# Performance work log

Hardware: AMD Instinct MI355X
Metric: run time of the kernel (lower is better)

Reference implementation:

```python
import jax, jax.numpy as jnp
import numpy as np

H = 512; W = 512; C = 32; B = 2; N = 120000; HEADS = 2; HD = C // HEADS; S = 9
INDEX_SHIFT = jnp.array([[0,0],[-1,0],[1,0],[0,1],[-1,1],[1,1],[0,-1],[-1,-1],[1,-1]], dtype=jnp.int32)


def setup_inputs() -> dict:
    key = jax.random.key(0)
    ks = jax.random.split(key, 20)
    bev_feats = jax.random.normal(ks[0], (B, N, C), jnp.float32)
    coors = []
    for b in range(B):
        perm = jax.random.permutation(ks[1 + b], H * W)[:N]
        coors.append(jnp.stack([perm // W, perm % W], axis=-1))
    bev_coors = jnp.stack(coors).astype(jnp.int32)
    s = 1.0 / np.sqrt(C)
    u = lambda k, shape, lim: jax.random.uniform(k, shape, jnp.float32, -lim, lim)
    return {
        'bev_feats': bev_feats,
        'bev_coors': bev_coors,
        'ln_w': jnp.ones((C,), jnp.float32),
        'ln_b': jnp.zeros((C,), jnp.float32),
        'wq': u(ks[3], (C, C), s), 'bq': u(ks[4], (C,), s),
        'wk': u(ks[5], (C, C), s), 'bk': u(ks[6], (C,), s),
        'wv': u(ks[7], (C, C), s), 'bv': u(ks[8], (C,), s),
        'pos_w': u(ks[9], (C, 2), 1.0 / np.sqrt(2.0)), 'pos_b': u(ks[10], (C,), 1.0 / np.sqrt(2.0)),
        'in_w': u(ks[11], (3 * C, C), s), 'in_b': jnp.zeros((3 * C,), jnp.float32),
        'out_w': u(ks[12], (C, C), s), 'out_b': jnp.zeros((C,), jnp.float32),
    }


def reference(bev_feats, bev_coors, ln_w, ln_b, wq, bq, wk, bk, wv, bv, pos_w, pos_b, in_w, in_b, out_w, out_b):
    def single(feats, coors):
        # LayerNorm (biased var, eps=1e-5)
        mu = feats.mean(-1, keepdims=True)
        var = feats.var(-1, keepdims=True)
        x = (feats - mu) / jnp.sqrt(var + 1e-5) * ln_w + ln_b
        # qkv 1x1 conv == linear
        q = x @ wq.T + bq
        k = x @ wk.T + bk
        v = x @ wv.T + bv
        # dense grid lookup: coord -> voxel index (-1 if empty)
        flat0 = coors[:, 0] * W + coors[:, 1]
        grid = jnp.full((H * W,), -1, jnp.int32).at[flat0].set(jnp.arange(N, dtype=jnp.int32))
        sc = coors[None] + INDEX_SHIFT[:, None]                      # [9,N,2]
        valid = (sc[..., 0] >= 0) & (sc[..., 0] < H) & (sc[..., 1] >= 0) & (sc[..., 1] < W)
        flat = jnp.clip(sc[..., 0], 0, H - 1) * W + jnp.clip(sc[..., 1], 0, W - 1)
        idx = jnp.where(valid, grid[flat], -1)                       # [9,N]
        pos = INDEX_SHIFT.astype(x.dtype) @ pos_w.T + pos_b          # [9,C]
        m = (idx >= 0)[..., None]
        tv = jnp.where(m, v[idx] + pos[:, None, :], 0.0)             # [9,N,C]
        tk = jnp.where(m, k[idx], 0.0)
        keyt = jnp.swapaxes(tk, 0, 1)                                # [N,9,C]
        valt = jnp.swapaxes(tv, 0, 1)
        # tiny MHA: query len 1, kv len 9, 2 heads (dropout inactive at eval)
        qp = q @ in_w[:C].T + in_b[:C]
        kp = keyt @ in_w[C:2 * C].T + in_b[C:2 * C]
        vp = valt @ in_w[2 * C:].T + in_b[2 * C:]
        qh = qp.reshape(N, HEADS, HD)
        kh = kp.reshape(N, S, HEADS, HD)
        vh = vp.reshape(N, S, HEADS, HD)
        attn = jax.nn.softmax(jnp.einsum('nhd,nshd->nhs', qh, kh) / np.sqrt(HD), axis=-1)
        o = jnp.einsum('nhs,nshd->nhd', attn, vh).reshape(N, C)
        o = o @ out_w.T + out_b
        # scatter to pseudo image [C,H,W]
        canvas = jnp.zeros((C, H * W), o.dtype).at[:, flat0].set(o.T)
        return canvas.reshape(C, H, W)
    return jax.vmap(single)(bev_feats, bev_coors)
```

## Files before the change

### kernel.cpp

```cpp
#include <hip/hip_runtime.h>
#include <hip/hip_fp16.h>
#include <cstdio>
#include <cstdint>

#define HH 512
#define WW 512
#define CC 32
#define BB 2
#define NN 120000
#define HWPIX (HH*WW)
#define NPTS (BB*NN)
#define NPIX (BB*HWPIX)
#define NBLK (NPIX/256)

__device__ __forceinline__ void h8_to_f8(float4 raw, float* o) {
    const __half2* h = (const __half2*)&raw;
    #pragma unroll
    for (int i = 0; i < 4; ++i) {
        float2 f = __half22float2(h[i]);
        o[2 * i] = f.x; o[2 * i + 1] = f.y;
    }
}

__global__ __launch_bounds__(256) void prep(const float* __restrict__ wq, const float* __restrict__ wk,
                          const float* __restrict__ wv, const float* __restrict__ in_w,
                          const float* __restrict__ out_w,
                          const float* __restrict__ bq, const float* __restrict__ bk,
                          const float* __restrict__ bv, const float* __restrict__ in_b,
                          const float* __restrict__ pos_w, const float* __restrict__ pos_b,
                          float* __restrict__ M, float* __restrict__ V, int* __restrict__ cnt) {
    int blk = blockIdx.x;
    if (blk < 16) {
        int tid = blk * 256 + threadIdx.x;
        int which = tid >> 10;
        int e = tid & 1023;
        int cp = e & 31;
        int j  = e >> 5;
        if (which < 3) {
            const float* w = (which == 0) ? wq : ((which == 1) ? wk : wv);
            const float* Wrow = in_w + (which * 32 + cp) * 32;
            float acc = 0.f;
            #pragma unroll
            for (int t = 0; t < 32; ++t) acc += Wrow[t] * w[t * 32 + j];
            M[which * 1024 + j * 32 + cp] = acc;
        } else {
            M[3 * 1024 + j * 32 + cp] = out_w[cp * 32 + j];
        }
    } else if (blk == 16) {
        int tid = threadIdx.x;
        if (tid < 32) {
            float a = 0.f, b = 0.f, c = 0.f;
            #pragma unroll
            for (int t = 0; t < 32; ++t) {
                a += in_w[tid * 32 + t] * bq[t];
                b += in_w[(32 + tid) * 32 + t] * bk[t];
                c += in_w[(64 + tid) * 32 + t] * bv[t];
            }
            V[tid]      = a + in_b[tid];
            V[32 + tid] = b;
            V[64 + tid] = c;
        } else if (tid < 128) {
            int grp = (tid - 32) >> 5;
            int cp  = tid & 31;
            float acc = 0.f;
            #pragma unroll
            for (int t = 0; t < 32; ++t) {
                float src = (grp == 0) ? pos_w[t * 2 + 0] : ((grp == 1) ? pos_w[t * 2 + 1] : pos_b[t]);
                acc += in_w[(64 + cp) * 32 + t] * src;
            }
            V[96 + grp * 32 + cp] = acc;
        }
    } else {
        for (int i = threadIdx.x; i < 2048; i += 256) cnt[i] = 0;
    }
}

__global__ void build_grid(const int* __restrict__ coors, int* __restrict__ grid,
                           int* __restrict__ cnt) {
    int P = blockIdx.x * blockDim.x + threadIdx.x;
    if (P >= NPTS) return;
    int b = P / NN;
    int n = P - b * NN;
    int y = coors[P * 2 + 0];
    int x = coors[P * 2 + 1];
    int pix = b * HWPIX + y * WW + x;
    grid[pix] = n;
    atomicAdd(&cnt[pix >> 8], 1);
}

__global__ __launch_bounds__(256) void scan2048(const int* __restrict__ cnt, int* __restrict__ off) {
    __shared__ int ps[256];
    int tid = threadIdx.x;
    int v[8], loc[8];
    int t = 0;
    #pragma unroll
    for (int k = 0; k < 8; ++k) { v[k] = cnt[tid * 8 + k]; loc[k] = t; t += v[k]; }
    ps[tid] = t;
    __syncthreads();
    for (int d = 1; d < 256; d <<= 1) {
        int val = ps[tid];
        int add = (tid >= d) ? ps[tid - d] : 0;
        __syncthreads();
        ps[tid] = val + add;
        __syncthreads();
    }
    int excl = (tid > 0) ? ps[tid - 1] : 0;
    #pragma unroll
    for (int k = 0; k < 8; ++k) off[tid * 8 + k] = excl + loc[k];
}

__global__ __launch_bounds__(256) void assign_ranks(const int* __restrict__ off,
                                                    int* __restrict__ grid,
                                                    int* __restrict__ rmap) {
    __shared__ int woff[4];
    int tid = threadIdx.x;
    int pix = blockIdx.x * 256 + tid;
    int n = grid[pix];
    bool occ = n >= 0;
    unsigned long long mask = __ballot(occ);
    int lane = tid & 63, wvi = tid >> 6;
    if (lane == 0) woff[wvi] = __popcll(mask);
    __syncthreads();
    int pre = 0;
    for (int w = 0; w < wvi; ++w) pre += woff[w];
    if (occ) {
        int r = off[blockIdx.x] + pre + __popcll(mask & ((1ull << lane) - 1ull));
        grid[pix] = r;
        rmap[(pix >> 18) * NN + n] = r;
    }
}

__global__ __launch_bounds__(128) void stage1(const float* __restrict__ feats,
                                              const float* __restrict__ ln_w,
                                              const float* __restrict__ ln_b,
                                              const float* __restrict__ M,
                                              const float* __restrict__ V,
                                              const int* __restrict__ rmap,
                                              __half* __restrict__ qh,
                                              __half* __restrict__ kvh) {
    int gp = blockIdx.x * 128 + threadIdx.x;
    int r = rmap[gp];

    const float* fr = feats + ((size_t)gp << 5);
    float x[32];
    #pragma unroll
    for (int k = 0; k < 8; ++k) ((float4*)x)[k] = ((const float4*)fr)[k];

    float s1 = 0.f, s2 = 0.f;
    #pragma unroll
    for (int j = 0; j < 32; ++j) { s1 += x[j]; s2 += x[j] * x[j]; }
    float mu   = s1 * (1.f / 32.f);
    float var  = s2 * (1.f / 32.f) - mu * mu;
    float rstd = rsqrtf(var + 1e-5f);
    #pragma unroll
    for (int j = 0; j < 32; ++j) x[j] = (x[j] - mu) * rstd * ln_w[j] + ln_b[j];

    float acc[32];
    __half2 hbuf[16];

    #pragma unroll
    for (int c = 0; c < 32; ++c) acc[c] = V[c];
    #pragma unroll
    for (int j = 0; j < 32; ++j) {
        float xv = x[j];
        #pragma unroll
        for (int c = 0; c < 32; ++c) acc[c] += xv * M[j * 32 + c];
    }
    #pragma unroll
    for (int c = 0; c < 16; ++c) hbuf[c] = __floats2half2_rn(acc[2 * c], acc[2 * c + 1]);
    {
        float4* qd = (float4*)(qh + ((size_t)r << 5));
        #pragma unroll
        for (int k = 0; k < 4; ++k) qd[k] = ((float4*)hbuf)[k];
    }

    __half2 kvbuf[32];

    #pragma unroll
    for (int c = 0; c < 32; ++c) acc[c] = V[32 + c];
    #pragma unroll
    for (int j = 0; j < 32; ++j) {
        float xv = x[j];
        #pragma unroll
        for (int c = 0; c < 32; ++c) acc[c] += xv * M[1024 + j * 32 + c];
    }
    #pragma unroll
    for (int c = 0; c < 16; ++c) kvbuf[c] = __floats2half2_rn(acc[2 * c], acc[2 * c + 1]);

    #pragma unroll
    for (int c = 0; c < 32; ++c) acc[c] = V[64 + c];
    #pragma unroll
    for (int j = 0; j < 32; ++j) {
        float xv = x[j];
        #pragma unroll
        for (int c = 0; c < 32; ++c) acc[c] += xv * M[2048 + j * 32 + c];
    }
    #pragma unroll
    for (int c = 0; c < 16; ++c) kvbuf[16 + c] = __floats2half2_rn(acc[2 * c], acc[2 * c + 1]);

    float4* kd = (float4*)(kvh + ((size_t)r << 6));
    #pragma unroll
    for (int k = 0; k < 8; ++k) kd[k] = ((float4*)kvbuf)[k];
}

__global__ __launch_bounds__(256) void stage23(const int* __restrict__ grid,
                                               const __half* __restrict__ qh,
                                               const __half* __restrict__ kvh,
                                               const float* __restrict__ M,
                                               const float* __restrict__ V,
                                               const float* __restrict__ in_b,
                                               const float* __restrict__ out_b,
                                               float* __restrict__ out) {
    __shared__ __half2 lso[256 * 17];
    __shared__ int lsr[256], lsp[256];
    __shared__ int woff[4];

    int w = (blockIdx.x & 7) * 256 + (blockIdx.x >> 3);
    int tid = threadIdx.x;
    int pix = w * 256 + tid;

    int rk = grid[pix];
    bool occ = rk >= 0;
    unsigned long long mask = __ballot(occ);
    int lane = tid & 63, wvi = tid >> 6;
    if (lane == 0) woff[wvi] = __popcll(mask);
    __syncthreads();
    int pre = 0;
    for (int ww = 0; ww < wvi; ++ww) pre += woff[ww];
    int cnt = woff[0] + woff[1] + woff[2] + woff[3];
    int slot = -1;
    if (occ) {
        slot = pre + __popcll(mask & ((1ull << lane) - 1ull));
        lsr[slot] = rk;
        lsp[slot] = tid;
    }
    __syncthreads();

    const int DYC[9] = {0,-1,1,0,-1,1,0,-1,1};
    const int DXC[9] = {0,0,0,1,1,1,-1,-1,-1};

    if (tid < cnt) {
        int i = tid;
        int r = lsr[i];
        int pixl = w * 256 + lsp[i];
        int b = pixl >> 18;
        int p = pixl & (HWPIX - 1);
        int y = p >> 9, x = p & 511;

        float qf[32];
        {
            const float4* q4 = (const float4*)(qh + ((size_t)r << 5));
            float4 r0 = q4[0], r1 = q4[1], r2 = q4[2], r3 = q4[3];
            h8_to_f8(r0, qf); h8_to_f8(r1, qf + 8); h8_to_f8(r2, qf + 16); h8_to_f8(r3, qf + 24);
        }

        int nr[9];
        #pragma unroll
        for (int s = 0; s < 9; ++s) {
            int sy = y + DYC[s], sx = x + DXC[s];
            nr[s] = (sy >= 0 && sy < HH && sx >= 0 && sx < WW) ? grid[(b << 18) + (sy << 9) + sx] : -1;
        }

        float eb0 = 0.f, eb1 = 0.f;
        #pragma unroll
        for (int c = 0; c < 16; ++c) {
            eb0 += qf[c]      * in_b[32 + c];
            eb1 += qf[16 + c] * in_b[48 + c];
        }

        float lg0[9], lg1[9];
        #pragma unroll
        for (int s = 0; s < 9; ++s) {
            float d0 = eb0, d1 = eb1;
            if (nr[s] >= 0) {
                const float4* kp = (const float4*)(kvh + ((size_t)nr[s] << 6));
                float kf[32];
                h8_to_f8(kp[0], kf);      h8_to_f8(kp[1], kf + 8);
                h8_to_f8(kp[2], kf + 16); h8_to_f8(kp[3], kf + 24);
                #pragma unroll
                for (int c = 0; c < 16; ++c) {
                    d0 += qf[c]      * kf[c];
                    d1 += qf[16 + c] * kf[16 + c];
                }
            }
            lg0[s] = d0 * 0.25f;
            lg1[s] = d1 * 0.25f;
        }
        float m0 = lg0[0], m1 = lg1[0];
        #pragma unroll
        for (int s = 1; s < 9; ++s) { m0 = fmaxf(m0, lg0[s]); m1 = fmaxf(m1, lg1[s]); }
        float l0 = 0.f, l1 = 0.f;
        #pragma unroll
        for (int s = 0; s < 9; ++s) {
            lg0[s] = __expf(lg0[s] - m0); l0 += lg0[s];
            lg1[s] = __expf(lg1[s] - m1); l1 += lg1[s];
        }

        float o[32];
        #pragma unroll
        for (int c = 0; c < 32; ++c) o[c] = 0.f;
        float wdy0 = 0.f, wdx0 = 0.f, woc0 = 0.f;
        float wdy1 = 0.f, wdx1 = 0.f, woc1 = 0.f;
        #pragma unroll
        for (int s = 0; s < 9; ++s) {
            if (nr[s] >= 0) {
                float w0 = lg0[s], w1 = lg1[s];
                const float4* vp = (const float4*)(kvh + ((size_t)nr[s] << 6)) + 4;
                float vf[32];
                h8_to_f8(vp[0], vf);      h8_to_f8(vp[1], vf + 8);
                h8_to_f8(vp[2], vf + 16); h8_to_f8(vp[3], vf + 24);
                #pragma unroll
                for (int c = 0; c < 16; ++c) {
                    o[c]      += w0 * vf[c];
                    o[16 + c] += w1 * vf[16 + c];
                }
                wdy0 += w0 * (float)DYC[s]; wdx0 += w0 * (float)DXC[s]; woc0 += w0;
                wdy1 += w1 * (float)DYC[s]; wdx1 += w1 * (float)DXC[s]; woc1 += w1;
            }
        }
        float rl0 = 1.f / l0, rl1 = 1.f / l1;
        #pragma unroll
        for (int c = 0; c < 16; ++c) {
            o[c]      = (o[c]      + wdy0 * V[96 + c]      + wdx0 * V[128 + c]      + woc0 * V[160 + c])      * rl0 + in_b[64 + c];
            o[16 + c] = (o[16 + c] + wdy1 * V[96 + 16 + c] + wdx1 * V[128 + 16 + c] + woc1 * V[160 + 16 + c]) * rl1 + in_b[80 + c];
        }

        float acc[32];
        #pragma unroll
        for (int c = 0; c < 32; ++c) acc[c] = out_b[c];
        #pragma unroll
        for (int j = 0; j < 32; ++j) {
            float vj = o[j];
            #pragma unroll
            for (int c = 0; c < 32; ++c) acc[c] += vj * M[3072 + j * 32 + c];
        }

        __half2* lrow = lso + i * 17;
        #pragma unroll
        for (int c = 0; c < 16; ++c) lrow[c] = __floats2half2_rn(acc[2 * c], acc[2 * c + 1]);
    }
    __syncthreads();

    int b = pix >> 18;
    int p = pix & (HWPIX - 1);
    float* outb = out + (size_t)b * CC * HWPIX + p;
    if (occ) {
        const __half2* lrow = lso + slot * 17;
        #pragma unroll
        for (int c2 = 0; c2 < 16; ++c2) {
            float2 f = __half22float2(lrow[c2]);
            outb[(2 * c2) * HWPIX]     = f.x;
            outb[(2 * c2 + 1) * HWPIX] = f.y;
        }
    } else {
        #pragma unroll
        for (int cc = 0; cc < 32; ++cc) outb[cc * HWPIX] = 0.f;
    }
}

extern "C" void kernel_launch(void* const* d_in, const int* in_sizes, int n_in,
                              void* d_out, int out_size, void* d_ws, size_t ws_size,
                              hipStream_t stream) {
    const float* feats = (const float*)d_in[0];
    const int*   coors = (const int*)d_in[1];
    const float* ln_w  = (const float*)d_in[2];
    const float* ln_b  = (const float*)d_in[3];
    const float* wq    = (const float*)d_in[4];
    const float* bq    = (const float*)d_in[5];
    const float* wk    = (const float*)d_in[6];
    const float* bk    = (const float*)d_in[7];
    const float* wv    = (const float*)d_in[8];
    const float* bv    = (const float*)d_in[9];
    const float* pos_w = (const float*)d_in[10];
    const float* pos_b = (const float*)d_in[11];
    const float* in_w  = (const float*)d_in[12];
    const float* in_b  = (const float*)d_in[13];
    const float* out_w = (const float*)d_in[14];
    const float* out_b = (const float*)d_in[15];

    int*    grid = (int*)d_ws;
    __half* qh   = (__half*)((int*)d_ws + NPIX);
    __half* kvh  = qh + (size_t)NPTS * 32;
    float*  M    = (float*)(kvh + (size_t)NPTS * 64);
    float*  V    = M + 4096;
    size_t need = (size_t)NPIX * 4 + (size_t)NPTS * 96 * 2 + (4096 + 192) * 4;
    if (ws_size < need) {
        fprintf(stderr, "kernel_launch: ws too small: %zu < %zu\n", ws_size, need);
        return;
    }
    int* cnt  = (int*)d_out + (out_size - 4096);
    int* off  = cnt + 2048;
    int* rmap = (int*)d_out + (out_size - 4096 - NPTS);

    hipMemsetAsync(grid, 0xFF, (size_t)NPIX * sizeof(int), stream);
    prep<<<18, 256, 0, stream>>>(wq, wk, wv, in_w, out_w, bq, bk, bv, in_b, pos_w, pos_b, M, V, cnt);
    build_grid<<<(NPTS + 255) / 256, 256, 0, stream>>>(coors, grid, cnt);
    scan2048<<<1, 256, 0, stream>>>(cnt, off);
    assign_ranks<<<NBLK, 256, 0, stream>>>(off, grid, rmap);
    stage1<<<NPTS / 128, 128, 0, stream>>>(feats, ln_w, ln_b, M, V, rmap, qh, kvh);
    stage23<<<NBLK, 256, 0, stream>>>(grid, qh, kvh, M, V, in_b, out_b, (float*)d_out);
}
```

Baseline: 237.1 us.

## Index q/kv by pixel with a byte occupancy map instead of compacted ranks

Removes the grid build, prefix-scan and rank-assignment kernels and the int grid memset. stage1 now reads coordinates directly and writes q and kv into pixel-indexed buffers, setting a byte occupancy flag per pixel; prep zeroes that flag map. stage23 tests neighbour occupancy with byte loads and fetches neighbour kv rows by pixel address, which keeps spatial neighbours close in memory. In exchange, the q/kv workspace grows to cover every pixel, so the data is sparse and cache lines are less densely used.

```diff
diff --git a/kernel.cpp b/kernel.cpp
--- a/kernel.cpp
+++ b/kernel.cpp
@@ -28,7 +28,7 @@
                           const float* __restrict__ bq, const float* __restrict__ bk,
                           const float* __restrict__ bv, const float* __restrict__ in_b,
                           const float* __restrict__ pos_w, const float* __restrict__ pos_b,
-                          float* __restrict__ M, float* __restrict__ V, int* __restrict__ cnt) {
+                          float* __restrict__ M, float* __restrict__ V, int* __restrict__ fmap_i) {
     int blk = blockIdx.x;
     if (blk < 16) {
         int tid = blk * 256 + threadIdx.x;
@@ -71,75 +71,27 @@
             V[96 + grp * 32 + cp] = acc;
         }
     } else {
-        for (int i = threadIdx.x; i < 2048; i += 256) cnt[i] = 0;
-    }
-}
-
-__global__ void build_grid(const int* __restrict__ coors, int* __restrict__ grid,
-                           int* __restrict__ cnt) {
-    int P = blockIdx.x * blockDim.x + threadIdx.x;
-    if (P >= NPTS) return;
-    int b = P / NN;
-    int n = P - b * NN;
-    int y = coors[P * 2 + 0];
-    int x = coors[P * 2 + 1];
-    int pix = b * HWPIX + y * WW + x;
-    grid[pix] = n;
-    atomicAdd(&cnt[pix >> 8], 1);
-}
-
-__global__ __launch_bounds__(256) void scan2048(const int* __restrict__ cnt, int* __restrict__ off) {
-    __shared__ int ps[256];
-    int tid = threadIdx.x;
-    int v[8], loc[8];
-    int t = 0;
-    #pragma unroll
-    for (int k = 0; k < 8; ++k) { v[k] = cnt[tid * 8 + k]; loc[k] = t; t += v[k]; }
-    ps[tid] = t;
-    __syncthreads();
-    for (int d = 1; d < 256; d <<= 1) {
-        int val = ps[tid];
-        int add = (tid >= d) ? ps[tid - d] : 0;
-        __syncthreads();
-        ps[tid] = val + add;
-        __syncthreads();
-    }
-    int excl = (tid > 0) ? ps[tid - 1] : 0;
-    #pragma unroll
-    for (int k = 0; k < 8; ++k) off[tid * 8 + k] = excl + loc[k];
-}
-
-__global__ __launch_bounds__(256) void assign_ranks(const int* __restrict__ off,
-                                                    int* __restrict__ grid,
-                                                    int* __restrict__ rmap) {
-    __shared__ int woff[4];
-    int tid = threadIdx.x;
-    int pix = blockIdx.x * 256 + tid;
-    int n = grid[pix];
-    bool occ = n >= 0;
-    unsigned long long mask = __ballot(occ);
-    int lane = tid & 63, wvi = tid >> 6;
-    if (lane == 0) woff[wvi] = __popcll(mask);
-    __syncthreads();
-    int pre = 0;
-    for (int w = 0; w < wvi; ++w) pre += woff[w];
-    if (occ) {
-        int r = off[blockIdx.x] + pre + __popcll(mask & ((1ull << lane) - 1ull));
-        grid[pix] = r;
-        rmap[(pix >> 18) * NN + n] = r;
-    }
-}
-
-__global__ __launch_bounds__(128) void stage1(const float* __restrict__ feats,
+        int base = (blk - 17) * 2048 + threadIdx.x * 8;
+        int4 z = {0, 0, 0, 0};
+        *(int4*)(fmap_i + base)     = z;
+        *(int4*)(fmap_i + base + 4) = z;
+    }
+}
+
+__global__ __launch_bounds__(256) void stage1(const float* __restrict__ feats,
+                                              const int* __restrict__ coors,
                                               const float* __restrict__ ln_w,
                                               const float* __restrict__ ln_b,
                                               const float* __restrict__ M,
                                               const float* __restrict__ V,
-                                              const int* __restrict__ rmap,
                                               __half* __restrict__ qh,
-                                              __half* __restrict__ kvh) {
-    int gp = blockIdx.x * 128 + threadIdx.x;
-    int r = rmap[gp];
+                                              __half* __restrict__ kvh,
+                                              unsigned char* __restrict__ fmap) {
+    int gp = blockIdx.x * 256 + threadIdx.x;
+    if (gp >= NPTS) return;
+    int b = (gp >= NN) ? 1 : 0;
+    int2 yx = ((const int2*)coors)[gp];
+    int pix = (b << 18) + (yx.x << 9) + yx.y;
 
     const float* fr = feats + ((size_t)gp << 5);
     float x[32];
@@ -169,7 +121,7 @@
     #pragma unroll
     for (int c = 0; c < 16; ++c) hbuf[c] = __floats2half2_rn(acc[2 * c], acc[2 * c + 1]);
     {
-        float4* qd = (float4*)(qh + ((size_t)r << 5));
+        float4* qd = (float4*)(qh + ((size_t)pix << 5));
         #pragma unroll
         for (int k = 0; k < 4; ++k) qd[k] = ((float4*)hbuf)[k];
     }
@@ -198,12 +150,14 @@
     #pragma unroll
     for (int c = 0; c < 16; ++c) kvbuf[16 + c] = __floats2half2_rn(acc[2 * c], acc[2 * c + 1]);
 
-    float4* kd = (float4*)(kvh + ((size_t)r << 6));
+    float4* kd = (float4*)(kvh + ((size_t)pix << 6));
     #pragma unroll
     for (int k = 0; k < 8; ++k) kd[k] = ((float4*)kvbuf)[k];
-}
-
-__global__ __launch_bounds__(256) void stage23(const int* __restrict__ grid,
+
+    fmap[pix] = 1;
+}
+
+__global__ __launch_bounds__(256) void stage23(const unsigned char* __restrict__ fmap,
                                                const __half* __restrict__ qh,
                                                const __half* __restrict__ kvh,
                                                const float* __restrict__ M,
@@ -212,15 +166,14 @@
                                                const float* __restrict__ out_b,
                                                float* __restrict__ out) {
     __shared__ __half2 lso[256 * 17];
-    __shared__ int lsr[256], lsp[256];
+    __shared__ int lsp[256];
     __shared__ int woff[4];
 
     int w = (blockIdx.x & 7) * 256 + (blockIdx.x >> 3);
     int tid = threadIdx.x;
     int pix = w * 256 + tid;
 
-    int rk = grid[pix];
-    bool occ = rk >= 0;
+    bool occ = fmap[pix] != 0;
     unsigned long long mask = __ballot(occ);
     int lane = tid & 63, wvi = tid >> 6;
     if (lane == 0) woff[wvi] = __popcll(mask);
@@ -231,7 +184,6 @@
     int slot = -1;
     if (occ) {
         slot = pre + __popcll(mask & ((1ull << lane) - 1ull));
-        lsr[slot] = rk;
         lsp[slot] = tid;
     }
     __syncthreads();
@@ -240,25 +192,27 @@
     const int DXC[9] = {0,0,0,1,1,1,-1,-1,-1};
 
     if (tid < cnt) {
-        int i = tid;
-        int r = lsr[i];
-        int pixl = w * 256 + lsp[i];
+        int pixl = w * 256 + lsp[tid];
         int b = pixl >> 18;
         int p = pixl & (HWPIX - 1);
         int y = p >> 9, x = p & 511;
 
         float qf[32];
         {
-            const float4* q4 = (const float4*)(qh + ((size_t)r << 5));
+            const float4* q4 = (const float4*)(qh + ((size_t)pixl << 5));
             float4 r0 = q4[0], r1 = q4[1], r2 = q4[2], r3 = q4[3];
             h8_to_f8(r0, qf); h8_to_f8(r1, qf + 8); h8_to_f8(r2, qf + 16); h8_to_f8(r3, qf + 24);
         }
 
-        int nr[9];
+        int np[9];
+        bool nv[9];
         #pragma unroll
         for (int s = 0; s < 9; ++s) {
             int sy = y + DYC[s], sx = x + DXC[s];
-            nr[s] = (sy >= 0 && sy < HH && sx >= 0 && sx < WW) ? grid[(b << 18) + (sy << 9) + sx] : -1;
+            bool inb = (sy >= 0) & (sy < HH) & (sx >= 0) & (sx < WW);
+            int npx = (b << 18) + (sy << 9) + sx;
+            np[s] = npx;
+            nv[s] = inb ? (fmap[npx] != 0) : false;
         }
 
         float eb0 = 0.f, eb1 = 0.f;
@@ -272,8 +226,8 @@
         #pragma unroll
         for (int s = 0; s < 9; ++s) {
             float d0 = eb0, d1 = eb1;
-            if (nr[s] >= 0) {
-                const float4* kp = (const float4*)(kvh + ((size_t)nr[s] << 6));
+            if (nv[s]) {
+                const float4* kp = (const float4*)(kvh + ((size_t)np[s] << 6));
                 float kf[32];
                 h8_to_f8(kp[0], kf);      h8_to_f8(kp[1], kf + 8);
                 h8_to_f8(kp[2], kf + 16); h8_to_f8(kp[3], kf + 24);
@@ -303,9 +257,9 @@
         float wdy1 = 0.f, wdx1 = 0.f, woc1 = 0.f;
         #pragma unroll
         for (int s = 0; s < 9; ++s) {
-            if (nr[s] >= 0) {
+            if (nv[s]) {
                 float w0 = lg0[s], w1 = lg1[s];
-                const float4* vp = (const float4*)(kvh + ((size_t)nr[s] << 6)) + 4;
+                const float4* vp = (const float4*)(kvh + ((size_t)np[s] << 6)) + 4;
                 float vf[32];
                 h8_to_f8(vp[0], vf);      h8_to_f8(vp[1], vf + 8);
                 h8_to_f8(vp[2], vf + 16); h8_to_f8(vp[3], vf + 24);
@@ -335,7 +289,7 @@
             for (int c = 0; c < 32; ++c) acc[c] += vj * M[3072 + j * 32 + c];
         }
 
-        __half2* lrow = lso + i * 17;
+        __half2* lrow = lso + tid * 17;
         #pragma unroll
         for (int c = 0; c < 16; ++c) lrow[c] = __floats2half2_rn(acc[2 * c], acc[2 * c + 1]);
     }
@@ -378,25 +332,19 @@
     const float* out_w = (const float*)d_in[14];
     const float* out_b = (const float*)d_in[15];
 
-    int*    grid = (int*)d_ws;
-    __half* qh   = (__half*)((int*)d_ws + NPIX);
-    __half* kvh  = qh + (size_t)NPTS * 32;
-    float*  M    = (float*)(kvh + (size_t)NPTS * 64);
+    float*  M    = (float*)d_ws;
     float*  V    = M + 4096;
-    size_t need = (size_t)NPIX * 4 + (size_t)NPTS * 96 * 2 + (4096 + 192) * 4;
+    __half* qh   = (__half*)(V + 192);
+    __half* kvh  = qh + (size_t)NPIX * 32;
+    unsigned char* fmap = (unsigned char*)(kvh + (size_t)NPIX * 64);
+    size_t need = (4096 + 192) * 4 + (size_t)NPIX * 96 * 2 + (size_t)NPIX;
     if (ws_size < need) {
         fprintf(stderr, "kernel_launch: ws too small: %zu < %zu\n", ws_size, need);
         return;
     }
-    int* cnt  = (int*)d_out + (out_size - 4096);
-    int* off  = cnt + 2048;
-    int* rmap = (int*)d_out + (out_size - 4096 - NPTS);
-
-    hipMemsetAsync(grid, 0xFF, (size_t)NPIX * sizeof(int), stream);
-    prep<<<18, 256, 0, stream>>>(wq, wk, wv, in_w, out_w, bq, bk, bv, in_b, pos_w, pos_b, M, V, cnt);
-    build_grid<<<(NPTS + 255) / 256, 256, 0, stream>>>(coors, grid, cnt);
-    scan2048<<<1, 256, 0, stream>>>(cnt, off);
-    assign_ranks<<<NBLK, 256, 0, stream>>>(off, grid, rmap);
-    stage1<<<NPTS / 128, 128, 0, stream>>>(feats, ln_w, ln_b, M, V, rmap, qh, kvh);
-    stage23<<<NBLK, 256, 0, stream>>>(grid, qh, kvh, M, V, in_b, out_b, (float*)d_out);
-}
+
+    prep<<<81, 256, 0, stream>>>(wq, wk, wv, in_w, out_w, bq, bk, bv, in_b, pos_w, pos_b,
+                                 M, V, (int*)fmap);
+    stage1<<<(NPTS + 255) / 256, 256, 0, stream>>>(feats, coors, ln_w, ln_b, M, V, qh, kvh, fmap);
+    stage23<<<NBLK, 256, 0, stream>>>(fmap, qh, kvh, M, V, in_b, out_b, (float*)d_out);
+}
```

Result: faster. 193.3 us (-18.5%).
